# Kernel tuning notes

Hardware: AMD Instinct MI355X
Metric: run time of the kernel (lower is better)

Reference implementation:

```python
import jax, jax.numpy as jnp
import numpy as np

VOCAB = 128

def setup_inputs() -> dict:
    key = jax.random.key(0)
    k1, k2, k3, k4 = jax.random.split(key, 4)
    B, S, H = 64, 512, 1024
    x = jax.random.randint(k1, (B, S), 0, VOCAB, dtype=jnp.int32)
    h = jnp.zeros((B, H), dtype=jnp.float32)
    # Xavier-normal-ish scaled params
    W_xh = jax.random.normal(k2, (VOCAB, H), dtype=jnp.float32) * (2.0 / (VOCAB + H)) ** 0.5
    W_hh = jax.random.normal(k3, (H, H), dtype=jnp.float32) * (1.0 / H) ** 0.5
    b_h = jnp.zeros((H,), dtype=jnp.float32)
    W_out = jax.random.normal(k4, (H, VOCAB), dtype=jnp.float32) * (1.0 / H) ** 0.5
    b_out = jnp.zeros((VOCAB,), dtype=jnp.float32)
    return {"x": x, "h": h, "W_xh": W_xh, "W_hh": W_hh, "b_h": b_h,
            "W_out": W_out, "b_out": b_out}

def reference(x, h, W_xh, W_hh, b_h, W_out, b_out):
    """x: (B,S) int32, h: (B,H). Returns (logits (B,S,V), h_final (B,H)).
    one_hot(x) @ W_xh == embedding gather W_xh[x] (same math, no dense one-hot).
    Dropout is identity (eval mode). Sequential tanh recurrence via lax.scan."""
    x_emb = W_xh[x]                      # (B, S, H) gather == one-hot matmul
    x_emb_t = jnp.swapaxes(x_emb, 0, 1)  # (S, B, H) scan over time

    def step(h, xe):
        h_new = jnp.tanh(xe + h @ W_hh + b_h)
        return h_new, h_new

    h_final, hidden = jax.lax.scan(step, h, x_emb_t)  # hidden: (S, B, H)
    hidden = jnp.swapaxes(hidden, 0, 1)               # (B, S, H)
    logits = hidden @ W_out + b_out                   # (B, S, V)
    return logits, h_final
```

## Files before the change

kernel.cpp:

```cpp
#include <hip/hip_runtime.h>
#include <hip/hip_bf16.h>
#include <stdint.h>


#define Bz 64
#define Sz 512
#define Hz 1024
#define Vz 128
#define NWG 64
#define COLS 32
#define WGT 512

typedef __attribute__((ext_vector_type(8)))  short short8;
typedef __attribute__((ext_vector_type(16))) float f32x16;
typedef __attribute__((ext_vector_type(4)))  unsigned u32x4;

__device__ __align__(16) unsigned short g_hfrag[3][2][64][64][8];
__device__ __align__(16) unsigned short g_hidden[(size_t)Sz*2*64*64*8];
__device__ __align__(16) unsigned short g_wout[64*4*64*8];

__device__ __forceinline__ unsigned short f2bf(float f) {
  union { float f; unsigned u; } v; v.f = f;
  unsigned r = v.u + 0x7FFFu + ((v.u >> 16) & 1u);
  return (unsigned short)(r >> 16);
}

__device__ __forceinline__ float fast_tanh(float x) {
  float cx = fminf(9.0f, fmaxf(-9.0f, x));
  float e  = __builtin_amdgcn_exp2f(cx * 2.88539008178f);
  return (e - 1.0f) * __builtin_amdgcn_rcpf(e + 1.0f);
}

__device__ __forceinline__ void load8_nodrain(const unsigned short* p0, u32x4 t[8]) {
  const unsigned short* p1 = p0 + 2048;
  asm volatile(
    "global_load_dwordx4 %0, %8, off sc1\n\t"
    "global_load_dwordx4 %1, %8, off offset:1024 sc1\n\t"
    "global_load_dwordx4 %2, %8, off offset:2048 sc1\n\t"
    "global_load_dwordx4 %3, %8, off offset:3072 sc1\n\t"
    "global_load_dwordx4 %4, %9, off sc1\n\t"
    "global_load_dwordx4 %5, %9, off offset:1024 sc1\n\t"
    "global_load_dwordx4 %6, %9, off offset:2048 sc1\n\t"
    "global_load_dwordx4 %7, %9, off offset:3072 sc1"
    : "=&v"(t[0]), "=&v"(t[1]), "=&v"(t[2]), "=&v"(t[3]),
      "=&v"(t[4]), "=&v"(t[5]), "=&v"(t[6]), "=&v"(t[7])
    : "v"(p0), "v"(p1)
    : "memory");
}

__device__ __forceinline__ void store16_sc1(unsigned short* p, u32x4 v) {
  asm volatile("global_store_dwordx4 %0, %1, off sc1" :: "v"(p), "v"(v) : "memory");
}
__device__ __forceinline__ void store4_sc1(unsigned short* p, unsigned v) {
  asm volatile("global_store_dword %0, %1, off sc1" :: "v"(p), "v"(v) : "memory");
}

__global__ void pack_wout(const float* __restrict__ W_out) {
  int gid = blockIdx.x * blockDim.x + threadIdx.x;
  int lane = gid & 63;
  int nt   = (gid >> 6) & 3;
  int kb   = gid >> 8;
  int n = nt * 32 + (lane & 31);
  int k0 = kb * 16 + (lane >> 5) * 8;
  unsigned short t[8];
#pragma unroll
  for (int j = 0; j < 8; ++j)
    t[j] = f2bf(W_out[(size_t)(k0 + j) * Vz + n]);
  uint4 w;
  w.x = (unsigned)t[0] | ((unsigned)t[1] << 16);
  w.y = (unsigned)t[2] | ((unsigned)t[3] << 16);
  w.z = (unsigned)t[4] | ((unsigned)t[5] << 16);
  w.w = (unsigned)t[6] | ((unsigned)t[7] << 16);
  *(uint4*)&g_wout[(size_t)gid * 8] = w;
}

__global__ __launch_bounds__(WGT) void rnn_persistent(
    const int* __restrict__ x, const float* __restrict__ h0,
    const float* __restrict__ W_xh, const float* __restrict__ W_hh,
    const float* __restrict__ b_h, float* __restrict__ out,
    unsigned* __restrict__ flags)
{
  __shared__ unsigned short ldsW[64 * 64 * 8];
  __shared__ float red[8 * 1024];

  const int g    = blockIdx.x;
  const int bh   = g >> 5;
  const int cg   = g & 31;
  const int n0g  = cg * COLS;
  const int tid  = threadIdx.x;
  const int lane = tid & 63;
  const int ki   = tid >> 6;
  const int bn   = lane & 31;

  for (int idx = tid; idx < 64 * 64; idx += WGT) {
    int kb = idx >> 6, L = idx & 63;
    int n = L & 31, kq = L >> 5;
    unsigned short t[8];
#pragma unroll
    for (int j = 0; j < 8; ++j)
      t[j] = f2bf(W_hh[(size_t)(kb * 16 + kq * 8 + j) * Hz + n0g + n]);
    uint4 w;
    w.x = (unsigned)t[0] | ((unsigned)t[1] << 16);
    w.y = (unsigned)t[2] | ((unsigned)t[3] << 16);
    w.z = (unsigned)t[4] | ((unsigned)t[5] << 16);
    w.w = (unsigned)t[6] | ((unsigned)t[7] << 16);
    *(uint4*)&ldsW[(size_t)idx * 8] = w;
  }

  if (tid < 128) {
    int s_idx = g * 128 + tid;
    int fbh = s_idx >> 12, fkb = (s_idx >> 6) & 63, fL = s_idx & 63;
    int m = fbh * 32 + (fL & 31);
    int k = fkb * 16 + (fL >> 5) * 8;
    const float* src = &h0[(size_t)m * Hz + k];
    float4 a0 = *(const float4*)&src[0];
    float4 a1 = *(const float4*)&src[4];
    u32x4 w;
    w.x = (unsigned)f2bf(a0.x) | ((unsigned)f2bf(a0.y) << 16);
    w.y = (unsigned)f2bf(a0.z) | ((unsigned)f2bf(a0.w) << 16);
    w.z = (unsigned)f2bf(a1.x) | ((unsigned)f2bf(a1.y) << 16);
    w.w = (unsigned)f2bf(a1.z) | ((unsigned)f2bf(a1.w) << 16);
    store16_sc1(&g_hfrag[0][fbh][fkb][fL][0], w);
  }

  __syncthreads();
  asm volatile("s_waitcnt vmcnt(0)" ::: "memory");
  if (lane == 0)
    __hip_atomic_store(&flags[(g * 8 + ki) * 4], 1u, __ATOMIC_RELAXED,
                       __HIP_MEMORY_SCOPE_AGENT);

  const int er   = tid & 31;
  const int em   = bh * 32 + er;
  const int c0   = (tid >> 5) * 2;
  const int kcol = n0g + c0;
  const int kb_g = kcol >> 4;
  const int kq2  = (kcol >> 3) & 1;
  const int lslot = kq2 * 32 + er;
  const size_t slotOff =
      (((size_t)bh * 64 + kb_g) * 64 + lslot) * 8 + (kcol & 7);
  const float bias0 = b_h[kcol], bias1 = b_h[kcol + 1];

  const int pflag =
      ((bh * 32 + ki * 4 + (lane >> 3)) * 8 + (lane & 7)) * 4;

  int tok_n = x[em * Sz];
  float2 xv_n = *(const float2*)&W_xh[(size_t)tok_n * Hz + kcol];

  int rp = 0;
  for (int s = 0; s < Sz; ++s) {
    const int wp = (rp == 2) ? 0 : rp + 1;
    const unsigned tgt = (unsigned)(s + 1);

    {
      for (int it = 0; it < 65536; ++it) {
        unsigned v = 0xFFFFFFFFu;
        if (lane < 32)
          v = __hip_atomic_load(&flags[pflag], __ATOMIC_RELAXED,
                                __HIP_MEMORY_SCOPE_AGENT);
        if (__all(v >= tgt)) break;
        __builtin_amdgcn_s_sleep(1);
      }
      asm volatile("" ::: "memory");
    }

    u32x4 t[8];
    load8_nodrain(&g_hfrag[rp][bh][ki * 8][lane][0], t);
    f32x16 acc0 = {}, acc1 = {};

#define STAGE(J, CNT)                                                          \
    {                                                                          \
      asm volatile("s_waitcnt vmcnt(" #CNT ")"                                 \
                   : "+v"(t[2 * (J)]), "+v"(t[2 * (J) + 1]));                  \
      const int kbp = ki * 8 + 2 * (J);                                        \
      short8 ba = *(const short8*)&ldsW[(size_t)(kbp * 64 + lane) * 8];        \
      short8 bb = *(const short8*)&ldsW[(size_t)((kbp + 1) * 64 + lane) * 8];  \
      acc0 = __builtin_amdgcn_mfma_f32_32x32x16_bf16(*(short8*)&t[2 * (J)],    \
                                                     ba, acc0, 0, 0, 0);       \
      acc1 = __builtin_amdgcn_mfma_f32_32x32x16_bf16(*(short8*)&t[2 * (J) + 1],\
                                                     bb, acc1, 0, 0, 0);       \
    }
    STAGE(0, 6) STAGE(1, 4) STAGE(2, 2) STAGE(3, 0)
#undef STAGE

    float2 xv = xv_n;
    if (s + 1 < Sz) {
      int t2 = x[em * Sz + s + 1];
      xv_n = *(const float2*)&W_xh[(size_t)t2 * Hz + kcol];
    }

    __syncthreads();
    {
#pragma unroll
      for (int r = 0; r < 16; ++r) {
        int m = 4 * (lane >> 5) + (r & 3) + 8 * (r >> 2);
        red[ki * 1024 + m * 32 + (bn ^ m)] = acc0[r] + acc1[r];
      }
    }
    __syncthreads();

    float z0, z1;
    {
      const int o0 = er * 32 + (c0 ^ er);
      const int o1 = er * 32 + ((c0 + 1) ^ er);
      z0 = ((red[o0] + red[1024 + o0]) + (red[2048 + o0] + red[3072 + o0])) +
           ((red[4096 + o0] + red[5120 + o0]) + (red[6144 + o0] + red[7168 + o0]));
      z1 = ((red[o1] + red[1024 + o1]) + (red[2048 + o1] + red[3072 + o1])) +
           ((red[4096 + o1] + red[5120 + o1]) + (red[6144 + o1] + red[7168 + o1]));
    }
    z0 = fast_tanh(z0 + xv.x + bias0);
    z1 = fast_tanh(z1 + xv.y + bias1);

    unsigned w2 = (unsigned)f2bf(z0) | ((unsigned)f2bf(z1) << 16);

    store4_sc1(&((unsigned short*)g_hfrag)[(size_t)wp * 65536 + slotOff], w2);
    asm volatile("s_waitcnt vmcnt(0)" ::: "memory");
    if (lane == 0)
      __hip_atomic_store(&flags[(g * 8 + ki) * 4], (unsigned)(s + 2),
                         __ATOMIC_RELAXED, __HIP_MEMORY_SCOPE_AGENT);

    *(unsigned*)&g_hidden[(size_t)s * 65536 + slotOff] = w2;
    if (s == Sz - 1) {
      float* hf = out + (size_t)Bz * Sz * Vz + (size_t)em * Hz + kcol;
      hf[0] = z0; hf[1] = z1;
    }
    rp = wp;
  }
}

__global__ __launch_bounds__(256) void logits_gemm(
    const float* __restrict__ b_out, float* __restrict__ out)
{
  const int tid = threadIdx.x, lane = tid & 63, nt = tid >> 6;
  const int s = blockIdx.x >> 1, mi = blockIdx.x & 1;
  const unsigned short* ab = &g_hidden[((size_t)s * 8192 + (size_t)mi * 4096) * 8];

  f32x16 acc = {};
#pragma unroll 8
  for (int kb = 0; kb < 64; ++kb) {
    short8 a = *(const short8*)&ab[(size_t)(kb * 64 + lane) * 8];
    short8 b = *(const short8*)&g_wout[(size_t)((kb * 4 + nt) * 64 + lane) * 8];
    acc = __builtin_amdgcn_mfma_f32_32x32x16_bf16(a, b, acc, 0, 0, 0);
  }
  const int col = nt * 32 + (lane & 31);
  const float bo = b_out[col];
  const int rbase = 4 * (lane >> 5);
#pragma unroll
  for (int r = 0; r < 16; ++r) {
    int m = rbase + (r & 3) + 8 * (r >> 2);
    int em = mi * 32 + m;
    out[((size_t)em * Sz + s) * Vz + col] = acc[r] + bo;
  }
}

extern "C" void kernel_launch(void* const* d_in, const int* in_sizes, int n_in,
                              void* d_out, int out_size, void* d_ws, size_t ws_size,
                              hipStream_t stream) {
  const int*   x     = (const int*)d_in[0];
  const float* h0    = (const float*)d_in[1];
  const float* W_xh  = (const float*)d_in[2];
  const float* W_hh  = (const float*)d_in[3];
  const float* b_h   = (const float*)d_in[4];
  const float* W_out = (const float*)d_in[5];
  const float* b_out = (const float*)d_in[6];
  float* out = (float*)d_out;

  (void)hipMemsetAsync(d_ws, 0, 8192, stream);
  pack_wout<<<64, 256, 0, stream>>>(W_out);
  rnn_persistent<<<NWG, WGT, 0, stream>>>(x, h0, W_xh, W_hh, b_h, out,
                                          (unsigned*)d_ws);
  logits_gemm<<<Sz * 2, 256, 0, stream>>>(b_out, out);
}
```

Baseline: 1.592 ms.

## Halve persistent workgroups to 32 and hold W_hh fragments in registers

New measurement: 1.803 ms. +13.3%, slower.

```diff
diff --git a/kernel.cpp b/kernel.cpp
--- a/kernel.cpp
+++ b/kernel.cpp
@@ -7,13 +7,14 @@
 #define Sz 512
 #define Hz 1024
 #define Vz 128
-#define NWG 64
-#define COLS 32
+#define NWG 32
+#define COLS 64
 #define WGT 512
 
 typedef __attribute__((ext_vector_type(8)))  short short8;
 typedef __attribute__((ext_vector_type(16))) float f32x16;
 typedef __attribute__((ext_vector_type(4)))  unsigned u32x4;
+typedef __attribute__((ext_vector_type(2)))  unsigned u32x2;
 
 __device__ __align__(16) unsigned short g_hfrag[3][2][64][64][8];
 __device__ __align__(16) unsigned short g_hidden[(size_t)Sz*2*64*64*8];
@@ -51,8 +52,8 @@
 __device__ __forceinline__ void store16_sc1(unsigned short* p, u32x4 v) {
   asm volatile("global_store_dwordx4 %0, %1, off sc1" :: "v"(p), "v"(v) : "memory");
 }
-__device__ __forceinline__ void store4_sc1(unsigned short* p, unsigned v) {
-  asm volatile("global_store_dword %0, %1, off sc1" :: "v"(p), "v"(v) : "memory");
+__device__ __forceinline__ void store8_sc1(unsigned short* p, u32x2 v) {
+  asm volatile("global_store_dwordx2 %0, %1, off sc1" :: "v"(p), "v"(v) : "memory");
 }
 
 __global__ void pack_wout(const float* __restrict__ W_out) {
@@ -80,35 +81,38 @@
     const float* __restrict__ b_h, float* __restrict__ out,
     unsigned* __restrict__ flags)
 {
-  __shared__ unsigned short ldsW[64 * 64 * 8];
-  __shared__ float red[8 * 1024];
+  __shared__ float red[24576];
 
   const int g    = blockIdx.x;
-  const int bh   = g >> 5;
-  const int cg   = g & 31;
+  const int bh   = g >> 4;
+  const int cg   = g & 15;
   const int n0g  = cg * COLS;
   const int tid  = threadIdx.x;
   const int lane = tid & 63;
   const int ki   = tid >> 6;
-  const int bn   = lane & 31;
-
-  for (int idx = tid; idx < 64 * 64; idx += WGT) {
-    int kb = idx >> 6, L = idx & 63;
-    int n = L & 31, kq = L >> 5;
-    unsigned short t[8];
-#pragma unroll
-    for (int j = 0; j < 8; ++j)
-      t[j] = f2bf(W_hh[(size_t)(kb * 16 + kq * 8 + j) * Hz + n0g + n]);
-    uint4 w;
-    w.x = (unsigned)t[0] | ((unsigned)t[1] << 16);
-    w.y = (unsigned)t[2] | ((unsigned)t[3] << 16);
-    w.z = (unsigned)t[4] | ((unsigned)t[5] << 16);
-    w.w = (unsigned)t[6] | ((unsigned)t[7] << 16);
-    *(uint4*)&ldsW[(size_t)idx * 8] = w;
-  }
-
-  if (tid < 128) {
-    int s_idx = g * 128 + tid;
+
+  short8 wf[2][8];
+  {
+#pragma unroll
+    for (int nt = 0; nt < 2; ++nt) {
+      const int col = n0g + nt * 32 + (lane & 31);
+      const float* wb = &W_hh[(size_t)(ki * 128 + (lane >> 5) * 8) * Hz + col];
+#pragma unroll
+      for (int p = 0; p < 8; ++p) {
+        const float* wp_ = wb + (size_t)p * 16 * Hz;
+        unsigned short tt[8];
+#pragma unroll
+        for (int j = 0; j < 8; ++j) tt[j] = f2bf(wp_[(size_t)j * Hz]);
+        short8 w;
+        w[0]=(short)tt[0]; w[1]=(short)tt[1]; w[2]=(short)tt[2]; w[3]=(short)tt[3];
+        w[4]=(short)tt[4]; w[5]=(short)tt[5]; w[6]=(short)tt[6]; w[7]=(short)tt[7];
+        wf[nt][p] = w;
+      }
+    }
+  }
+
+  if (tid < 256) {
+    int s_idx = g * 256 + tid;
     int fbh = s_idx >> 12, fkb = (s_idx >> 6) & 63, fL = s_idx & 63;
     int m = fbh * 32 + (fL & 31);
     int k = fkb * 16 + (fL >> 5) * 8;
@@ -123,7 +127,6 @@
     store16_sc1(&g_hfrag[0][fbh][fkb][fL][0], w);
   }
 
-  __syncthreads();
   asm volatile("s_waitcnt vmcnt(0)" ::: "memory");
   if (lane == 0)
     __hip_atomic_store(&flags[(g * 8 + ki) * 4], 1u, __ATOMIC_RELAXED,
@@ -131,20 +134,21 @@
 
   const int er   = tid & 31;
   const int em   = bh * 32 + er;
-  const int c0   = (tid >> 5) * 2;
+  const int jc   = tid >> 5;
+  const int c0   = jc * 4;
   const int kcol = n0g + c0;
   const int kb_g = kcol >> 4;
   const int kq2  = (kcol >> 3) & 1;
   const int lslot = kq2 * 32 + er;
   const size_t slotOff =
       (((size_t)bh * 64 + kb_g) * 64 + lslot) * 8 + (kcol & 7);
-  const float bias0 = b_h[kcol], bias1 = b_h[kcol + 1];
+  float4 bias = *(const float4*)&b_h[kcol];
 
   const int pflag =
-      ((bh * 32 + ki * 4 + (lane >> 3)) * 8 + (lane & 7)) * 4;
+      ((bh * 16 + ki * 2 + (lane >> 3)) * 8 + (lane & 7)) * 4;
 
   int tok_n = x[em * Sz];
-  float2 xv_n = *(const float2*)&W_xh[(size_t)tok_n * Hz + kcol];
+  float4 xv_n = *(const float4*)&W_xh[(size_t)tok_n * Hz + kcol];
 
   int rp = 0;
   for (int s = 0; s < Sz; ++s) {
@@ -152,9 +156,10 @@
     const unsigned tgt = (unsigned)(s + 1);
 
     {
-      for (int it = 0; it < 65536; ++it) {
+      const int bound = (s == 0) ? 131072 : 16384;
+      for (int it = 0; it < bound; ++it) {
         unsigned v = 0xFFFFFFFFu;
-        if (lane < 32)
+        if (lane < 16)
           v = __hip_atomic_load(&flags[pflag], __ATOMIC_RELAXED,
                                 __HIP_MEMORY_SCOPE_AGENT);
         if (__all(v >= tgt)) break;
@@ -167,25 +172,22 @@
     load8_nodrain(&g_hfrag[rp][bh][ki * 8][lane][0], t);
     f32x16 acc0 = {}, acc1 = {};
 
-#define STAGE(J, CNT)                                                          \
+#define STAGE(P, CNT)                                                          \
     {                                                                          \
-      asm volatile("s_waitcnt vmcnt(" #CNT ")"                                 \
-                   : "+v"(t[2 * (J)]), "+v"(t[2 * (J) + 1]));                  \
-      const int kbp = ki * 8 + 2 * (J);                                        \
-      short8 ba = *(const short8*)&ldsW[(size_t)(kbp * 64 + lane) * 8];        \
-      short8 bb = *(const short8*)&ldsW[(size_t)((kbp + 1) * 64 + lane) * 8];  \
-      acc0 = __builtin_amdgcn_mfma_f32_32x32x16_bf16(*(short8*)&t[2 * (J)],    \
-                                                     ba, acc0, 0, 0, 0);       \
-      acc1 = __builtin_amdgcn_mfma_f32_32x32x16_bf16(*(short8*)&t[2 * (J) + 1],\
-                                                     bb, acc1, 0, 0, 0);       \
-    }
-    STAGE(0, 6) STAGE(1, 4) STAGE(2, 2) STAGE(3, 0)
+      asm volatile("s_waitcnt vmcnt(" #CNT ")" : "+v"(t[(P)]));                \
+      acc0 = __builtin_amdgcn_mfma_f32_32x32x16_bf16(*(short8*)&t[(P)],        \
+                                                     wf[0][(P)], acc0, 0, 0, 0);\
+      acc1 = __builtin_amdgcn_mfma_f32_32x32x16_bf16(*(short8*)&t[(P)],        \
+                                                     wf[1][(P)], acc1, 0, 0, 0);\
+    }
+    STAGE(0, 7) STAGE(1, 6) STAGE(2, 5) STAGE(3, 4)
+    STAGE(4, 3) STAGE(5, 2) STAGE(6, 1) STAGE(7, 0)
 #undef STAGE
 
-    float2 xv = xv_n;
+    float4 xv = xv_n;
     if (s + 1 < Sz) {
       int t2 = x[em * Sz + s + 1];
-      xv_n = *(const float2*)&W_xh[(size_t)t2 * Hz + kcol];
+      xv_n = *(const float4*)&W_xh[(size_t)t2 * Hz + kcol];
     }
 
     __syncthreads();
@@ -193,35 +195,42 @@
 #pragma unroll
       for (int r = 0; r < 16; ++r) {
         int m = 4 * (lane >> 5) + (r & 3) + 8 * (r >> 2);
-        red[ki * 1024 + m * 32 + (bn ^ m)] = acc0[r] + acc1[r];
+        int cA = (lane & 31);
+        int cB = 32 + (lane & 31);
+        red[ki * 2048 + m * 64 + (cA ^ m)] = acc0[r];
+        red[ki * 2048 + m * 64 + (cB ^ m)] = acc1[r];
       }
     }
     __syncthreads();
 
-    float z0, z1;
-    {
-      const int o0 = er * 32 + (c0 ^ er);
-      const int o1 = er * 32 + ((c0 + 1) ^ er);
-      z0 = ((red[o0] + red[1024 + o0]) + (red[2048 + o0] + red[3072 + o0])) +
-           ((red[4096 + o0] + red[5120 + o0]) + (red[6144 + o0] + red[7168 + o0]));
-      z1 = ((red[o1] + red[1024 + o1]) + (red[2048 + o1] + red[3072 + o1])) +
-           ((red[4096 + o1] + red[5120 + o1]) + (red[6144 + o1] + red[7168 + o1]));
-    }
-    z0 = fast_tanh(z0 + xv.x + bias0);
-    z1 = fast_tanh(z1 + xv.y + bias1);
-
-    unsigned w2 = (unsigned)f2bf(z0) | ((unsigned)f2bf(z1) << 16);
-
-    store4_sc1(&((unsigned short*)g_hfrag)[(size_t)wp * 65536 + slotOff], w2);
+    float z[4];
+#pragma unroll
+    for (int j = 0; j < 4; ++j) {
+      const int off = er * 64 + ((c0 + j) ^ er);
+      z[j] = ((red[off] + red[2048 + off]) + (red[4096 + off] + red[6144 + off])) +
+             ((red[8192 + off] + red[10240 + off]) +
+              (red[12288 + off] + red[14336 + off]));
+    }
+    z[0] = fast_tanh(z[0] + xv.x + bias.x);
+    z[1] = fast_tanh(z[1] + xv.y + bias.y);
+    z[2] = fast_tanh(z[2] + xv.z + bias.z);
+    z[3] = fast_tanh(z[3] + xv.w + bias.w);
+
+    u32x2 w2;
+    w2.x = (unsigned)f2bf(z[0]) | ((unsigned)f2bf(z[1]) << 16);
+    w2.y = (unsigned)f2bf(z[2]) | ((unsigned)f2bf(z[3]) << 16);
+
+    store8_sc1(&((unsigned short*)g_hfrag)[(size_t)wp * 65536 + slotOff], w2);
     asm volatile("s_waitcnt vmcnt(0)" ::: "memory");
     if (lane == 0)
       __hip_atomic_store(&flags[(g * 8 + ki) * 4], (unsigned)(s + 2),
                          __ATOMIC_RELAXED, __HIP_MEMORY_SCOPE_AGENT);
 
-    *(unsigned*)&g_hidden[(size_t)s * 65536 + slotOff] = w2;
+    *(u32x2*)&g_hidden[(size_t)s * 65536 + slotOff] = w2;
     if (s == Sz - 1) {
       float* hf = out + (size_t)Bz * Sz * Vz + (size_t)em * Hz + kcol;
-      hf[0] = z0; hf[1] = z1;
+      float4 f0 = {z[0], z[1], z[2], z[3]};
+      *(float4*)hf = f0;
     }
     rp = wp;
   }
```
